# Kernel tuning notes

Hardware: AMD Instinct MI355X
Metric: run time of the kernel (lower is better)

The kernel has to match this reference:

```python
import jax, jax.numpy as jnp
import numpy as np

B, S, HID = 2, 2048, 1024
H, HKV, D = 16, 16, 64


def _rope_tables(seq_len, dim, base=10000.0):
    inv_freq = 1.0 / (base ** (np.arange(0, dim, 2, dtype=np.float32) / dim))
    t = np.arange(seq_len, dtype=np.float32)
    freqs = np.outer(t, inv_freq)            # [S, D/2]
    emb = np.concatenate([freqs, freqs], axis=-1)  # [S, D]
    return jnp.asarray(np.cos(emb)), jnp.asarray(np.sin(emb))


def setup_inputs() -> dict:
    key = jax.random.key(0)
    k1, k2, k3 = jax.random.split(key, 3)
    hidden_states = jax.random.normal(k1, (B, S, HID), dtype=jnp.float32)
    cos, sin = _rope_tables(S, D)
    w_qkv = jax.random.normal(k2, ((H + 2 * HKV) * D, HID), dtype=jnp.float32) / np.sqrt(HID)
    w_o = jax.random.normal(k3, (HID, H * D), dtype=jnp.float32) / np.sqrt(H * D)
    return {"hidden_states": hidden_states, "cos": cos, "sin": sin, "w_qkv": w_qkv, "w_o": w_o}


def _rotate_half(x):
    mid = x.shape[-1] // 2
    return jnp.concatenate([-x[..., mid:], x[..., :mid]], axis=-1)


def reference(hidden_states, cos, sin, w_qkv, w_o):
    b, s, _ = hidden_states.shape
    qkv = hidden_states @ w_qkv.T                       # [B,S,(H+2HKV)*D]
    qkv = qkv.reshape(b, s, H + 2 * HKV, D).transpose(0, 2, 1, 3)  # [B,heads,S,D]
    q, k, v = qkv[:, :H], qkv[:, H:H + HKV], qkv[:, H + HKV:]
    # RoPE (cos/sin broadcast [S,D] -> [B,H,S,D])
    q = q * cos + _rotate_half(q) * sin
    k = k * cos + _rotate_half(k) * sin
    # causal SDPA
    scale = 1.0 / jnp.sqrt(jnp.asarray(D, dtype=q.dtype))
    scores = jnp.einsum("bhqd,bhkd->bhqk", q, k) * scale
    causal = jnp.tril(jnp.ones((s, s), dtype=bool))
    scores = jnp.where(causal, scores, jnp.finfo(scores.dtype).min)
    attn = jax.nn.softmax(scores, axis=-1)
    out = jnp.einsum("bhqk,bhkd->bhqd", attn, v)        # [B,H,S,D]
    out = out.transpose(0, 2, 1, 3).reshape(b, s, H * D)
    return out @ w_o.T
```

## Files before the change

### kernel.cpp

```cpp
#include <hip/hip_runtime.h>

typedef __bf16 bf16_t;
typedef __bf16 bf16x8 __attribute__((ext_vector_type(8)));
typedef __bf16 bf16x4 __attribute__((ext_vector_type(4)));
typedef float  f32x4  __attribute__((ext_vector_type(4)));

#define LOG2E 1.44269504088896340736f

__device__ __forceinline__ void gload_lds16(const void* g, void* l) {
  __builtin_amdgcn_global_load_lds(
      (const __attribute__((address_space(1))) void*)g,
      (__attribute__((address_space(3))) void*)l, 16, 0, 0);
}

__device__ __forceinline__ void store_c(float* p, float v)  { *p = v; }
__device__ __forceinline__ void store_c(bf16_t* p, float v) { *p = (bf16_t)v; }

__global__ __launch_bounds__(256) void cast_kernel(const float* __restrict__ in,
                                                   bf16_t* __restrict__ out, int n4) {
  int i = blockIdx.x * 256 + threadIdx.x;
  const int stride = gridDim.x * 256;
  for (; i < n4; i += stride) {
    f32x4 v = *(const f32x4*)(in + (size_t)i * 4);
    bf16x4 o;
#pragma unroll
    for (int j = 0; j < 4; ++j) o[j] = (bf16_t)v[j];
    *(bf16x4*)(out + (size_t)i * 4) = o;
  }
}

template <typename OutT>
__global__ __launch_bounds__(256) void gemm_bt(const bf16_t* __restrict__ A,
                                               const bf16_t* __restrict__ B,
                                               OutT* __restrict__ C,
                                               int M, int N, int K) {
  __shared__ bf16_t As[128 * 32];
  __shared__ bf16_t Bs[128 * 32];
  const int tid  = threadIdx.x;
  const int lane = tid & 63;
  const int wid  = tid >> 6;
  const int wm = wid >> 1, wn = wid & 1;
  const size_t m0 = (size_t)blockIdx.y * 128;
  const size_t n0 = (size_t)blockIdx.x * 128;

  f32x4 acc[4][4] = {};

  for (int k0 = 0; k0 < K; k0 += 32) {
#pragma unroll
    for (int j = 0; j < 2; ++j) {
      const int c = tid + j * 256;
      const int r = c >> 2;
      const int kp = (c & 3) * 8;
      gload_lds16(A + (m0 + r) * K + k0 + kp, As + (size_t)c * 8);
      gload_lds16(B + (n0 + r) * K + k0 + kp, Bs + (size_t)c * 8);
    }
    __syncthreads();

    const int kk = (lane >> 4) * 8;
    const int rs = lane & 15;
    bf16x8 af[4], bfv[4];
#pragma unroll
    for (int t = 0; t < 4; ++t) {
      af[t]  = *(const bf16x8*)(As + (wm * 64 + t * 16 + rs) * 32 + kk);
      bfv[t] = *(const bf16x8*)(Bs + (wn * 64 + t * 16 + rs) * 32 + kk);
    }
#pragma unroll
    for (int mt = 0; mt < 4; ++mt)
#pragma unroll
      for (int nt = 0; nt < 4; ++nt)
        acc[mt][nt] = __builtin_amdgcn_mfma_f32_16x16x32_bf16(af[mt], bfv[nt], acc[mt][nt], 0, 0, 0);
    __syncthreads();
  }

#pragma unroll
  for (int mt = 0; mt < 4; ++mt)
#pragma unroll
    for (int nt = 0; nt < 4; ++nt)
#pragma unroll
      for (int r = 0; r < 4; ++r) {
        size_t row = m0 + wm * 64 + mt * 16 + (lane >> 4) * 4 + r;
        size_t col = n0 + wn * 64 + nt * 16 + (lane & 15);
        store_c(C + row * N + col, acc[mt][nt][r]);
      }
}

__global__ __launch_bounds__(256) void rope_reorg(const bf16_t* __restrict__ qkv,
                                                  const float* __restrict__ cosT,
                                                  const float* __restrict__ sinT,
                                                  bf16_t* __restrict__ Q,
                                                  bf16_t* __restrict__ Kd,
                                                  bf16_t* __restrict__ Vt) {
  __shared__ bf16_t T[64 * 72];
  const int blk  = blockIdx.x;
  const int sblk = blk & 31;
  const int hh   = (blk >> 5) % 48;
  const int b    = blk / (32 * 48);
  const int s0   = sblk * 64;
  const int tid  = threadIdx.x;

  if (hh < 32) {
    const bool isq = hh < 16;
    const int h = isq ? hh : hh - 16;
    bf16_t* dst = (isq ? Q : Kd) + (size_t)(b * 16 + h) * 2048 * 64;
    for (int u = tid; u < 512; u += 256) {
      const int s = u >> 3, oct = u & 7;
      const size_t src = ((size_t)(b * 2048) + s0 + s) * 3072 + hh * 64;
      bf16x8 x = *(const bf16x8*)(qkv + src + oct * 8);
      bf16x8 y = *(const bf16x8*)(qkv + src + ((oct * 8) ^ 32));
      const float* cp = cosT + (size_t)(s0 + s) * 64 + oct * 8;
      const float* sp = sinT + (size_t)(s0 + s) * 64 + oct * 8;
      const float sgn = (oct < 4) ? -1.f : 1.f;
      bf16x8 ov;
#pragma unroll
      for (int j = 0; j < 8; ++j) {
        float xv = (float)x[j], yv = (float)y[j];
        ov[j] = (bf16_t)(xv * cp[j] + sgn * yv * sp[j]);
      }
      *(bf16x8*)(dst + (size_t)(s0 + s) * 64 + oct * 8) = ov;
    }
  } else {
    const int hv = hh - 32;
    for (int u = tid; u < 512; u += 256) {
      const int s = u >> 3, oct = u & 7;
      *(bf16x8*)(&T[s * 72 + oct * 8]) =
          *(const bf16x8*)(qkv + ((size_t)(b * 2048) + s0 + s) * 3072 + hh * 64 + oct * 8);
    }
    __syncthreads();
    bf16_t* dst = Vt + (size_t)(b * 16 + hv) * 64 * 2048;
    for (int u = tid; u < 512; u += 256) {
      const int d = u >> 3, soct = u & 7;
      bf16x8 w;
#pragma unroll
      for (int j = 0; j < 8; ++j) w[j] = T[(soct * 8 + j) * 72 + d];
      *(bf16x8*)(dst + (size_t)d * 2048 + s0 + soct * 8) = w;
    }
  }
}

__global__ __launch_bounds__(256) void attn_kernel(const bf16_t* __restrict__ Q,
                                                   const bf16_t* __restrict__ Kt,
                                                   const bf16_t* __restrict__ Vt,
                                                   bf16_t* __restrict__ O) {
  const int qblk = blockIdx.x;
  const int h    = blockIdx.y;
  const int b    = blockIdx.z;
  const int tid  = threadIdx.x;
  const int lane = tid & 63;
  const int wid  = tid >> 6;
  const int bh   = b * 16 + h;
  const bf16_t* Qb = Q  + (size_t)bh * 2048 * 64;
  const bf16_t* Kb = Kt + (size_t)bh * 2048 * 64;
  const bf16_t* Vb = Vt + (size_t)bh * 64 * 2048;

  __shared__ bf16_t Ks[32 * 72];
  __shared__ bf16_t Vs[64 * 56];
  __shared__ bf16_t Ps[4][16 * 40];

  const int q0  = qblk * 64 + wid * 16;
  const int l15 = lane & 15;
  const int dd  = (lane >> 4) * 8;

  bf16x8 qf0 = *(const bf16x8*)(Qb + (size_t)(q0 + l15) * 64 + dd);
  bf16x8 qf1 = *(const bf16x8*)(Qb + (size_t)(q0 + l15) * 64 + 32 + dd);

  f32x4 o[4] = {};
  float mr[4], lr[4];
#pragma unroll
  for (int r = 0; r < 4; ++r) { mr[r] = -3.0e38f; lr[r] = 0.f; }

  const int nkv = qblk * 64 + 64;
  const int ks_row = tid >> 3, ks_oct = tid & 7;
  const int vs_row = tid >> 2, vs_oct = tid & 3;

  for (int kv0 = 0; kv0 < nkv; kv0 += 32) {
    *(bf16x8*)(Ks + ks_row * 72 + ks_oct * 8) =
        *(const bf16x8*)(Kb + (size_t)(kv0 + ks_row) * 64 + ks_oct * 8);
    *(bf16x8*)(Vs + vs_row * 56 + vs_oct * 8) =
        *(const bf16x8*)(Vb + (size_t)vs_row * 2048 + kv0 + vs_oct * 8);
    __syncthreads();

    f32x4 st[2] = {};
#pragma unroll
    for (int kt = 0; kt < 2; ++kt) {
      bf16x8 kf0 = *(const bf16x8*)(Ks + (kt * 16 + l15) * 72 + dd);
      bf16x8 kf1 = *(const bf16x8*)(Ks + (kt * 16 + l15) * 72 + 32 + dd);
      st[kt] = __builtin_amdgcn_mfma_f32_16x16x32_bf16(qf0, kf0, st[kt], 0, 0, 0);
      st[kt] = __builtin_amdgcn_mfma_f32_16x16x32_bf16(qf1, kf1, st[kt], 0, 0, 0);
    }

    float p[2][4];
    const bool need_mask = (kv0 + 31 > q0);
#pragma unroll
    for (int kt = 0; kt < 2; ++kt)
#pragma unroll
      for (int r = 0; r < 4; ++r) {
        float v = st[kt][r] * 0.125f;
        if (need_mask) {
          int kg = kv0 + kt * 16 + l15;
          int qg = q0 + (lane >> 4) * 4 + r;
          if (kg > qg) v = -3.0e38f;
        }
        p[kt][r] = v;
      }

    float al[4];
#pragma unroll
    for (int r = 0; r < 4; ++r) {
      float mb = fmaxf(p[0][r], p[1][r]);
      mb = fmaxf(mb, __shfl_xor(mb, 1));
      mb = fmaxf(mb, __shfl_xor(mb, 2));
      mb = fmaxf(mb, __shfl_xor(mb, 4));
      mb = fmaxf(mb, __shfl_xor(mb, 8));
      float mn = fmaxf(mr[r], mb);
      al[r] = exp2f((mr[r] - mn) * LOG2E);
      float s0 = exp2f((p[0][r] - mn) * LOG2E);
      float s1 = exp2f((p[1][r] - mn) * LOG2E);
      p[0][r] = s0; p[1][r] = s1;
      float lb = s0 + s1;
      lb += __shfl_xor(lb, 1);
      lb += __shfl_xor(lb, 2);
      lb += __shfl_xor(lb, 4);
      lb += __shfl_xor(lb, 8);
      lr[r] = lr[r] * al[r] + lb;
      mr[r] = mn;
    }
#pragma unroll
    for (int dt = 0; dt < 4; ++dt)
#pragma unroll
      for (int r = 0; r < 4; ++r) o[dt][r] *= al[r];

#pragma unroll
    for (int kt = 0; kt < 2; ++kt)
#pragma unroll
      for (int r = 0; r < 4; ++r)
        Ps[wid][((lane >> 4) * 4 + r) * 40 + kt * 16 + l15] = (bf16_t)p[kt][r];

    asm volatile("s_waitcnt lgkmcnt(0)" ::: "memory");
    __builtin_amdgcn_sched_barrier(0);

    bf16x8 pa = *(const bf16x8*)(&Ps[wid][l15 * 40 + dd]);
#pragma unroll
    for (int dt = 0; dt < 4; ++dt) {
      bf16x8 vf = *(const bf16x8*)(Vs + (dt * 16 + l15) * 56 + dd);
      o[dt] = __builtin_amdgcn_mfma_f32_16x16x32_bf16(pa, vf, o[dt], 0, 0, 0);
    }
    __syncthreads();
  }

#pragma unroll
  for (int r = 0; r < 4; ++r) {
    float inv = 1.f / lr[r];
    size_t srow = (size_t)b * 2048 + q0 + (lane >> 4) * 4 + r;
#pragma unroll
    for (int dt = 0; dt < 4; ++dt)
      O[srow * 1024 + h * 64 + dt * 16 + l15] = (bf16_t)(o[dt][r] * inv);
  }
}

extern "C" void kernel_launch(void* const* d_in, const int* in_sizes, int n_in,
                              void* d_out, int out_size, void* d_ws, size_t ws_size,
                              hipStream_t stream) {
  const float* hs   = (const float*)d_in[0];
  const float* cosT = (const float*)d_in[1];
  const float* sinT = (const float*)d_in[2];
  const float* wqkv = (const float*)d_in[3];
  const float* wo   = (const float*)d_in[4];
  float* out = (float*)d_out;

  char* ws = (char*)d_ws;
  bf16_t* hs_b   = (bf16_t*)(ws);
  bf16_t* wqkv_b = (bf16_t*)(ws + 8388608);
  bf16_t* wo_b   = (bf16_t*)(ws + 14680064);
  bf16_t* qkv    = (bf16_t*)(ws + 16777216);
  bf16_t* Qb     = (bf16_t*)(ws + 41943040);
  bf16_t* Kb     = (bf16_t*)(ws + 50331648);
  bf16_t* Vtb    = (bf16_t*)(ws + 58720256);
  bf16_t* aout   = (bf16_t*)(ws + 67108864);

  cast_kernel<<<2048, 256, 0, stream>>>(hs,   hs_b,   4194304 / 4);
  cast_kernel<<<1024, 256, 0, stream>>>(wqkv, wqkv_b, 3145728 / 4);
  cast_kernel<<<512,  256, 0, stream>>>(wo,   wo_b,   1048576 / 4);

  gemm_bt<bf16_t><<<dim3(24, 32), 256, 0, stream>>>(hs_b, wqkv_b, qkv, 4096, 3072, 1024);

  rope_reorg<<<3072, 256, 0, stream>>>(qkv, cosT, sinT, Qb, Kb, Vtb);

  attn_kernel<<<dim3(32, 16, 2), 256, 0, stream>>>(Qb, Kb, Vtb, aout);

  gemm_bt<float><<<dim3(8, 32), 256, 0, stream>>>(aout, wo_b, out, 4096, 1024, 1024);
}
```

Baseline: 334.5 us.

## Drop shared K/V staging in attention, use per-wave causal bounds and reversed block order

The attention kernel no longer stages K and V tiles through shared memory behind block-wide barriers. Each wave now loads its K and V fragments straight from global memory, in 64-key steps, and skips 16-key sub-tiles beyond its own last query row. Query blocks are launched in reverse order so the heaviest causal blocks start first, and the softmax scale is folded into a single fma before a native exp2. This removes the __syncthreads and the redundant masked work, but waves in a block now fetch the same K/V separately, relying on cache, and register pressure rises.

```diff
diff --git a/kernel.cpp b/kernel.cpp
--- a/kernel.cpp
+++ b/kernel.cpp
@@ -141,7 +141,7 @@
                                                    const bf16_t* __restrict__ Kt,
                                                    const bf16_t* __restrict__ Vt,
                                                    bf16_t* __restrict__ O) {
-  const int qblk = blockIdx.x;
+  const int qblk = 31 - blockIdx.x;
   const int h    = blockIdx.y;
   const int b    = blockIdx.z;
   const int tid  = threadIdx.x;
@@ -152,13 +152,14 @@
   const bf16_t* Kb = Kt + (size_t)bh * 2048 * 64;
   const bf16_t* Vb = Vt + (size_t)bh * 64 * 2048;
 
-  __shared__ bf16_t Ks[32 * 72];
-  __shared__ bf16_t Vs[64 * 56];
-  __shared__ bf16_t Ps[4][16 * 40];
+  __shared__ bf16_t Ps[4][16 * 72];
 
   const int q0  = qblk * 64 + wid * 16;
   const int l15 = lane & 15;
-  const int dd  = (lane >> 4) * 8;
+  const int g   = lane >> 4;
+  const int dd  = g * 8;
+  const int qmax = q0 + 15;
+  const float SC = 0.125f * LOG2E;
 
   bf16x8 qf0 = *(const bf16x8*)(Qb + (size_t)(q0 + l15) * 64 + dd);
   bf16x8 qf1 = *(const bf16x8*)(Qb + (size_t)(q0 + l15) * 64 + 32 + dd);
@@ -168,55 +169,62 @@
 #pragma unroll
   for (int r = 0; r < 4; ++r) { mr[r] = -3.0e38f; lr[r] = 0.f; }
 
-  const int nkv = qblk * 64 + 64;
-  const int ks_row = tid >> 3, ks_oct = tid & 7;
-  const int vs_row = tid >> 2, vs_oct = tid & 3;
-
-  for (int kv0 = 0; kv0 < nkv; kv0 += 32) {
-    *(bf16x8*)(Ks + ks_row * 72 + ks_oct * 8) =
-        *(const bf16x8*)(Kb + (size_t)(kv0 + ks_row) * 64 + ks_oct * 8);
-    *(bf16x8*)(Vs + vs_row * 56 + vs_oct * 8) =
-        *(const bf16x8*)(Vb + (size_t)vs_row * 2048 + kv0 + vs_oct * 8);
-    __syncthreads();
-
-    f32x4 st[2] = {};
-#pragma unroll
-    for (int kt = 0; kt < 2; ++kt) {
-      bf16x8 kf0 = *(const bf16x8*)(Ks + (kt * 16 + l15) * 72 + dd);
-      bf16x8 kf1 = *(const bf16x8*)(Ks + (kt * 16 + l15) * 72 + 32 + dd);
-      st[kt] = __builtin_amdgcn_mfma_f32_16x16x32_bf16(qf0, kf0, st[kt], 0, 0, 0);
-      st[kt] = __builtin_amdgcn_mfma_f32_16x16x32_bf16(qf1, kf1, st[kt], 0, 0, 0);
-    }
-
-    float p[2][4];
-    const bool need_mask = (kv0 + 31 > q0);
-#pragma unroll
-    for (int kt = 0; kt < 2; ++kt)
-#pragma unroll
-      for (int r = 0; r < 4; ++r) {
-        float v = st[kt][r] * 0.125f;
-        if (need_mask) {
-          int kg = kv0 + kt * 16 + l15;
-          int qg = q0 + (lane >> 4) * 4 + r;
-          if (kg > qg) v = -3.0e38f;
+  for (int kv0 = 0; kv0 <= qmax; kv0 += 64) {
+    f32x4 st[4];
+    bool act[4];
+#pragma unroll
+    for (int kt = 0; kt < 4; ++kt) {
+      act[kt] = (kv0 + kt * 16 <= qmax);
+      if (act[kt]) {
+        const bf16_t* kp = Kb + (size_t)(kv0 + kt * 16 + l15) * 64;
+        bf16x8 kf0 = *(const bf16x8*)(kp + dd);
+        bf16x8 kf1 = *(const bf16x8*)(kp + 32 + dd);
+        f32x4 acc = {};
+        acc = __builtin_amdgcn_mfma_f32_16x16x32_bf16(qf0, kf0, acc, 0, 0, 0);
+        acc = __builtin_amdgcn_mfma_f32_16x16x32_bf16(qf1, kf1, acc, 0, 0, 0);
+        st[kt] = acc;
+      }
+    }
+
+    const bool need_mask = (kv0 + 63 > q0);
+    if (need_mask) {
+#pragma unroll
+      for (int kt = 0; kt < 4; ++kt) {
+        if (!act[kt]) continue;
+#pragma unroll
+        for (int r = 0; r < 4; ++r) {
+          const int kg = kv0 + kt * 16 + l15;
+          const int qg = q0 + g * 4 + r;
+          if (kg > qg) st[kt][r] = -3.0e38f;
         }
-        p[kt][r] = v;
-      }
-
+      }
+    }
+
+    float p[4][4];
     float al[4];
 #pragma unroll
     for (int r = 0; r < 4; ++r) {
-      float mb = fmaxf(p[0][r], p[1][r]);
+      float mb = -3.0e38f;
+#pragma unroll
+      for (int kt = 0; kt < 4; ++kt)
+        if (act[kt]) mb = fmaxf(mb, st[kt][r]);
       mb = fmaxf(mb, __shfl_xor(mb, 1));
       mb = fmaxf(mb, __shfl_xor(mb, 2));
       mb = fmaxf(mb, __shfl_xor(mb, 4));
       mb = fmaxf(mb, __shfl_xor(mb, 8));
-      float mn = fmaxf(mr[r], mb);
-      al[r] = exp2f((mr[r] - mn) * LOG2E);
-      float s0 = exp2f((p[0][r] - mn) * LOG2E);
-      float s1 = exp2f((p[1][r] - mn) * LOG2E);
-      p[0][r] = s0; p[1][r] = s1;
-      float lb = s0 + s1;
+      const float mn = fmaxf(mr[r], mb);
+      al[r] = __builtin_amdgcn_exp2f((mr[r] - mn) * SC);
+      const float mc = mn * SC;
+      float lb = 0.f;
+#pragma unroll
+      for (int kt = 0; kt < 4; ++kt) {
+        if (act[kt]) {
+          p[kt][r] = __builtin_amdgcn_exp2f(__builtin_fmaf(st[kt][r], SC, -mc));
+          lb += p[kt][r];
+        } else {
+          p[kt][r] = 0.f;
+        }
+      }
       lb += __shfl_xor(lb, 1);
       lb += __shfl_xor(lb, 2);
       lb += __shfl_xor(lb, 4);
@@ -230,27 +238,30 @@
       for (int r = 0; r < 4; ++r) o[dt][r] *= al[r];
 
 #pragma unroll
-    for (int kt = 0; kt < 2; ++kt)
+    for (int kt = 0; kt < 4; ++kt)
 #pragma unroll
       for (int r = 0; r < 4; ++r)
-        Ps[wid][((lane >> 4) * 4 + r) * 40 + kt * 16 + l15] = (bf16_t)p[kt][r];
+        Ps[wid][(g * 4 + r) * 72 + kt * 16 + l15] = (bf16_t)p[kt][r];
 
     asm volatile("s_waitcnt lgkmcnt(0)" ::: "memory");
     __builtin_amdgcn_sched_barrier(0);
 
-    bf16x8 pa = *(const bf16x8*)(&Ps[wid][l15 * 40 + dd]);
-#pragma unroll
-    for (int dt = 0; dt < 4; ++dt) {
-      bf16x8 vf = *(const bf16x8*)(Vs + (dt * 16 + l15) * 56 + dd);
-      o[dt] = __builtin_amdgcn_mfma_f32_16x16x32_bf16(pa, vf, o[dt], 0, 0, 0);
-    }
-    __syncthreads();
+#pragma unroll
+    for (int half = 0; half < 2; ++half) {
+      if (kv0 + half * 32 > qmax) break;
+      bf16x8 pa = *(const bf16x8*)(&Ps[wid][l15 * 72 + half * 32 + dd]);
+#pragma unroll
+      for (int dt = 0; dt < 4; ++dt) {
+        bf16x8 vf = *(const bf16x8*)(Vb + (size_t)(dt * 16 + l15) * 2048 + kv0 + half * 32 + dd);
+        o[dt] = __builtin_amdgcn_mfma_f32_16x16x32_bf16(pa, vf, o[dt], 0, 0, 0);
+      }
+    }
   }
 
 #pragma unroll
   for (int r = 0; r < 4; ++r) {
-    float inv = 1.f / lr[r];
-    size_t srow = (size_t)b * 2048 + q0 + (lane >> 4) * 4 + r;
+    const float inv = 1.f / lr[r];
+    size_t srow = (size_t)b * 2048 + q0 + g * 4 + r;
 #pragma unroll
     for (int dt = 0; dt < 4; ++dt)
       O[srow * 1024 + h * 64 + dt * 16 + l15] = (bf16_t)(o[dt][r] * inv);
```

New measurement: 381.0 us. 1.14x slower.
